# Kernel tuning notes

Hardware: AMD Instinct MI355X
Metric: run time of the kernel (lower is better)

The kernel has to match this reference:

```python
import jax, jax.numpy as jnp
import numpy as np

N, D, E = 32768, 128, 524288
B, L = 64, 512          # 64 graphs of 512 nodes
H, DH = 8, 16           # heads, head dim


def setup_inputs() -> dict:
    key = jax.random.key(0)
    ks = jax.random.split(key, 16)
    s = 0.02
    w = lambda k, shape: (jax.random.normal(k, shape, jnp.float32) * s)
    z = lambda *shape: jnp.zeros(shape, jnp.float32)
    o = lambda *shape: jnp.ones(shape, jnp.float32)
    return {
        "x": jax.random.normal(ks[0], (N, D), jnp.float32),
        "edge_index": jax.random.randint(ks[1], (2, E), 0, N, jnp.int32),
        "eps": jnp.zeros(()),
        "W_loc1": w(ks[2], (D, 2 * D)), "b_loc1": z(2 * D),
        "W_loc2": w(ks[3], (2 * D, D)), "b_loc2": z(D),
        "g1": o(D), "beta1": z(D),
        "Wq": w(ks[4], (D, D)), "bq": z(D),
        "Wk": w(ks[5], (D, D)), "bk": z(D),
        "Wv": w(ks[6], (D, D)), "bv": z(D),
        "Wo": w(ks[7], (D, D)), "bo": z(D),
        "g2": o(D), "beta2": z(D),
        "Wf1": w(ks[8], (D, 2 * D)), "bf1": z(2 * D),
        "Wf2": w(ks[9], (2 * D, D)), "bf2": z(D),
        "g3": o(D), "beta3": z(D),
    }


def _bn(x, g, b):
    # BatchNorm1d, training mode: batch stats over the node dimension
    m = x.mean(0)
    v = x.var(0)
    return (x - m) * jax.lax.rsqrt(v + 1e-5) * g + b


def reference(x, edge_index, eps, W_loc1, b_loc1, W_loc2, b_loc2, g1, beta1,
              Wq, bq, Wk, bk, Wv, bv, Wo, bo, g2, beta2,
              Wf1, bf1, Wf2, bf2, g3, beta3):
    src, dst = edge_index[0], edge_index[1]
    # --- local MPNN (GIN): sum-aggregate neighbours then MLP ---
    agg = jax.ops.segment_sum(x[src], dst, num_segments=N)          # [N, D]
    h = (1.0 + eps) * x + agg
    h = jax.nn.relu(h @ W_loc1 + b_loc1) @ W_loc2 + b_loc2
    h_local = _bn(x + h, g1, beta1)
    # --- global attention over each graph's (permuted) node sequence ---
    xd = x.reshape(B, L, D)
    q = (xd @ Wq + bq).reshape(B, L, H, DH)
    k = (xd @ Wk + bk).reshape(B, L, H, DH)
    v = (xd @ Wv + bv).reshape(B, L, H, DH)
    scores = jnp.einsum("blhd,bmhd->bhlm", q, k) / np.sqrt(DH)
    attn = jax.nn.softmax(scores, axis=-1)
    o = jnp.einsum("bhlm,bmhd->blhd", attn, v).reshape(B, L, D)
    o = (o @ Wo + bo).reshape(N, D)
    h_attn = _bn(x + o, g2, beta2)
    # --- combine + FFN block ---
    h = h_local + h_attn
    f = jax.nn.relu(h @ Wf1 + bf1) @ Wf2 + bf2
    return _bn(h + f, g3, beta3)
```

## Files before the change

kernel.cpp:

```cpp
#include <hip/hip_runtime.h>
#include <cstdint>
#include <cstddef>

typedef unsigned short u16;
typedef unsigned int u32;

using short8 = __attribute__((ext_vector_type(8))) short;
using f32x4  = __attribute__((ext_vector_type(4))) float;

__device__ __forceinline__ float b2f(u16 v) {
  union { u32 u; float f; } c; c.u = ((u32)v) << 16; return c.f;
}
__device__ __forceinline__ u16 f2b(float f) {
  union { float f; u32 u; } c; c.f = f;
  u32 u = c.u;
  u += 0x7fffu + ((u >> 16) & 1u);
  return (u16)(u >> 16);
}

__global__ __launch_bounds__(256)
void f2bf_kernel(const float* __restrict__ in, u16* __restrict__ outp) {
  int i = blockIdx.x * 256 + threadIdx.x;
  float2 v = *(const float2*)(in + (size_t)i * 2);
  *(u32*)(outp + (size_t)i * 2) = (u32)f2b(v.x) | ((u32)f2b(v.y) << 16);
}

__global__ __launch_bounds__(256)
void prep_kernel(const float* __restrict__ Wl1, const float* __restrict__ Wl2,
                 const float* __restrict__ Wq,  const float* __restrict__ Wk,
                 const float* __restrict__ Wv,  const float* __restrict__ Wo,
                 const float* __restrict__ Wf1, const float* __restrict__ Wf2,
                 const float* __restrict__ bl1, const float* __restrict__ bl2,
                 const float* __restrict__ bq,  const float* __restrict__ bk,
                 const float* __restrict__ bv,  const float* __restrict__ bo,
                 const float* __restrict__ bf1, const float* __restrict__ bf2,
                 u16* __restrict__ Bt, float* __restrict__ biasAll) {
  int idx = blockIdx.x * 256 + threadIdx.x;
  if (idx < 196608) {
    const float* W; int local, ks, N;
    if      (idx <  32768) { W = Wl1; local = idx;          ks = 7; N = 256; }
    else if (idx <  65536) { W = Wl2; local = idx - 32768;  ks = 8; N = 128; }
    else if (idx <  81920) { W = Wq;  local = idx - 65536;  ks = 7; N = 128; }
    else if (idx <  98304) { W = Wk;  local = idx - 81920;  ks = 7; N = 128; }
    else if (idx < 114688) { W = Wv;  local = idx - 98304;  ks = 7; N = 128; }
    else if (idx < 131072) { W = Wo;  local = idx - 114688; ks = 7; N = 128; }
    else if (idx < 163840) { W = Wf1; local = idx - 131072; ks = 7; N = 256; }
    else                   { W = Wf2; local = idx - 163840; ks = 8; N = 128; }
    int n = local >> ks, k = local & ((1 << ks) - 1);
    Bt[idx] = f2b(W[(size_t)k * N + n]);
  }
  int t = idx - 196608;
  if (t >= 0 && t < 1280) {
    float v;
    if      (t <  256) v = bl1[t];
    else if (t <  384) v = bl2[t - 256];
    else if (t <  512) v = bq[t - 384];
    else if (t <  640) v = bk[t - 512];
    else if (t <  768) v = bv[t - 640];
    else if (t <  896) v = bo[t - 768];
    else if (t < 1152) v = bf1[t - 896];
    else               v = bf2[t - 1152];
    biasAll[t] = v;
  }
}

__global__ void hist_kernel(const int* __restrict__ dst, int* __restrict__ deg, int E) {
  int i = blockIdx.x * 256 + threadIdx.x;
  if (i < E) atomicAdd(&deg[dst[i]], 1);
}

__global__ __launch_bounds__(256)
void scan1_kernel(const int* __restrict__ deg, int* __restrict__ bsum) {
  int t = threadIdx.x, b = blockIdx.x;
  int v = deg[b * 256 + t];
#pragma unroll
  for (int off = 1; off < 64; off <<= 1) v += __shfl_xor(v, off);
  __shared__ int wsum[4];
  if ((t & 63) == 0) wsum[t >> 6] = v;
  __syncthreads();
  if (t == 0) bsum[b] = wsum[0] + wsum[1] + wsum[2] + wsum[3];
}

__global__ void scan2_kernel(const int* __restrict__ bsum, int* __restrict__ boff,
                             int* __restrict__ rowptrN) {
  __shared__ int sh[128];
  int t = threadIdx.x;
  int v = bsum[t];
  sh[t] = v;
  __syncthreads();
  for (int off = 1; off < 128; off <<= 1) {
    int u = (t >= off) ? sh[t - off] : 0;
    __syncthreads();
    sh[t] += u;
    __syncthreads();
  }
  boff[t] = sh[t] - v;
  if (t == 127) *rowptrN = sh[127];
}

__global__ __launch_bounds__(256)
void scan3_kernel(const int* __restrict__ deg, const int* __restrict__ boff,
                  int* __restrict__ rowptr, int* __restrict__ cursor) {
  __shared__ int sh[256];
  int t = threadIdx.x, b = blockIdx.x;
  int idx = b * 256 + t;
  int v = deg[idx];
  sh[t] = v;
  __syncthreads();
  for (int off = 1; off < 256; off <<= 1) {
    int u = (t >= off) ? sh[t - off] : 0;
    __syncthreads();
    sh[t] += u;
    __syncthreads();
  }
  int ex = sh[t] - v + boff[b];
  rowptr[idx] = ex;
  cursor[idx] = ex;
}

__global__ void scatter_kernel(const int* __restrict__ src, const int* __restrict__ dst,
                               int* __restrict__ cursor, int* __restrict__ csr, int E) {
  int i = blockIdx.x * 256 + threadIdx.x;
  if (i < E) {
    int d = dst[i];
    int pos = atomicAdd(&cursor[d], 1);
    csr[pos] = src[i];
  }
}

__global__ __launch_bounds__(256)
void agg_kernel(const u16* __restrict__ xb, const float* __restrict__ x,
                const int* __restrict__ csr, const int* __restrict__ rowptr,
                const float* __restrict__ eps, u16* __restrict__ hin, int N) {
  int node = blockIdx.x * 4 + (threadIdx.x >> 6);
  if (node >= N) return;
  int lane = threadIdx.x & 63;
  float ep1 = 1.0f + eps[0];
  int s0 = rowptr[node], s1 = rowptr[node + 1];
  float a0 = 0.f, a1 = 0.f;
  int e = s0;
  for (; e + 4 <= s1; e += 4) {
    int i0 = csr[e], i1 = csr[e + 1], i2 = csr[e + 2], i3 = csr[e + 3];
    u32 w0 = *(const u32*)(xb + (size_t)i0 * 128 + lane * 2);
    u32 w1 = *(const u32*)(xb + (size_t)i1 * 128 + lane * 2);
    u32 w2 = *(const u32*)(xb + (size_t)i2 * 128 + lane * 2);
    u32 w3 = *(const u32*)(xb + (size_t)i3 * 128 + lane * 2);
    a0 += b2f((u16)w0) + b2f((u16)w1) + b2f((u16)w2) + b2f((u16)w3);
    a1 += b2f((u16)(w0 >> 16)) + b2f((u16)(w1 >> 16))
        + b2f((u16)(w2 >> 16)) + b2f((u16)(w3 >> 16));
  }
  for (; e < s1; e++) {
    int s = csr[e];
    u32 w = *(const u32*)(xb + (size_t)s * 128 + lane * 2);
    a0 += b2f((u16)w);
    a1 += b2f((u16)(w >> 16));
  }
  float2 xw = *(const float2*)(x + (size_t)node * 128 + lane * 2);
  a0 += ep1 * xw.x;
  a1 += ep1 * xw.y;
  *(u32*)(hin + (size_t)node * 128 + lane * 2) = (u32)f2b(a0) | ((u32)f2b(a1) << 16);
}

__global__ __launch_bounds__(256)
void gemm_fast(const u16* __restrict__ A, const u16* __restrict__ Bt,
               const float* __restrict__ bias, const float* __restrict__ residf,
               const u16* __restrict__ residb,
               u16* __restrict__ C0, u16* __restrict__ C1, u16* __restrict__ C2,
               float* __restrict__ ssum, float* __restrict__ ssq,
               int K, int ntshift, int relu, float scale0, int headmajor) {
  const int tid = threadIdx.x, wave = tid >> 6, lane = tid & 63;
  const int quad = lane >> 4, c = lane & 15;
  const int y = blockIdx.y;
  const int ti = y >> ntshift, nt = y & ((1 << ntshift) - 1);
  const int Nout = 32 << ntshift;
  const u16* Btp = Bt + (size_t)ti * Nout * K;
  const float* bp = bias + ti * Nout;
  u16* C = (ti == 0) ? C0 : ((ti == 1) ? C1 : C2);
  const float scl = (ti == 0) ? scale0 : 1.0f;
  const int row0 = blockIdx.x * 128 + wave * 32;
  const int col0 = nt * 32;

  const u16* Ap0 = A   + (size_t)(row0 + c) * K + quad * 8;
  const u16* Ap1 = Ap0 + (size_t)16 * K;
  const u16* Bp0 = Btp + (size_t)(col0 + c) * K + quad * 8;
  const u16* Bp1 = Bp0 + (size_t)16 * K;

  f32x4 acc[2][2];
#pragma unroll
  for (int i = 0; i < 2; i++)
#pragma unroll
    for (int j = 0; j < 2; j++)
#pragma unroll
      for (int r = 0; r < 4; r++) acc[i][j][r] = 0.f;

#pragma unroll 4
  for (int kc = 0; kc < K; kc += 32) {
    short8 a0 = *(const short8*)(Ap0 + kc);
    short8 a1 = *(const short8*)(Ap1 + kc);
    short8 b0 = *(const short8*)(Bp0 + kc);
    short8 b1 = *(const short8*)(Bp1 + kc);
    acc[0][0] = __builtin_amdgcn_mfma_f32_16x16x32_bf16(a0, b0, acc[0][0], 0, 0, 0);
    acc[0][1] = __builtin_amdgcn_mfma_f32_16x16x32_bf16(a0, b1, acc[0][1], 0, 0, 0);
    acc[1][0] = __builtin_amdgcn_mfma_f32_16x16x32_bf16(a1, b0, acc[1][0], 0, 0, 0);
    acc[1][1] = __builtin_amdgcn_mfma_f32_16x16x32_bf16(a1, b1, acc[1][1], 0, 0, 0);
  }

#pragma unroll
  for (int ci = 0; ci < 2; ci++) {
    int col = col0 + ci * 16 + c;
    float bv = bp[col];
    float sp = 0.f, qp = 0.f;
#pragma unroll
    for (int mi = 0; mi < 2; mi++) {
#pragma unroll
      for (int r = 0; r < 4; r++) {
        int m = row0 + mi * 16 + quad * 4 + r;
        float v = acc[mi][ci][r] + bv;
        if (relu) v = fmaxf(v, 0.f);
        if (residf) v += residf[(size_t)m * Nout + col];
        else if (residb) v += b2f(residb[(size_t)m * Nout + col]);
        v *= scl;
        size_t cidx;
        if (headmajor) {
          int bb = m >> 9, j = m & 511;
          cidx = (size_t)(bb * 8 + (col >> 4)) * 8192 + (size_t)j * 16 + (col & 15);
        } else {
          cidx = (size_t)m * Nout + col;
        }
        C[cidx] = f2b(v);
        sp += v; qp += v * v;
      }
    }
    if (ssum) {
      sp += __shfl_xor(sp, 16); sp += __shfl_xor(sp, 32);
      qp += __shfl_xor(qp, 16); qp += __shfl_xor(qp, 32);
      if (quad == 0) {
        atomicAdd(&ssum[col], sp);
        atomicAdd(&ssq[col], qp);
      }
    }
  }
}

__global__ __launch_bounds__(512)
void attn_kernel(const u16* __restrict__ Q, const u16* __restrict__ Km,
                 const u16* __restrict__ Vm, u16* __restrict__ O) {
  __shared__ __align__(16) u16 Ksh[512 * 24];
  __shared__ __align__(16) u16 Vt[16 * 520];
  __shared__ __align__(16) u16 Psh[8][16 * 40];
  const int bh = blockIdx.x >> 1, qhalf = blockIdx.x & 1;
  const int b = bh >> 3, hh = bh & 7;
  const size_t qkvbase = (size_t)bh * 8192;
  const size_t obase   = (size_t)b * 512 * 128 + hh * 16;
  const int tid = threadIdx.x;

  {
    int j = tid;
    short8 k0 = *(const short8*)(Km + qkvbase + (size_t)j * 16);
    short8 k1 = *(const short8*)(Km + qkvbase + (size_t)j * 16 + 8);
    short8 v0 = *(const short8*)(Vm + qkvbase + (size_t)j * 16);
    short8 v1 = *(const short8*)(Vm + qkvbase + (size_t)j * 16 + 8);
    *(short8*)&Ksh[j * 24]     = k0;
    *(short8*)&Ksh[j * 24 + 8] = k1;
    int jl = j & 31;
    int j2 = (j & ~31) | (((jl & 15) << 1) | (jl >> 4));
#pragma unroll
    for (int t = 0; t < 8; t++) Vt[t * 520 + j2] = (u16)v0[t];
#pragma unroll
    for (int t = 0; t < 8; t++) Vt[(8 + t) * 520 + j2] = (u16)v1[t];
  }
  __syncthreads();

  const int wave = tid >> 6, lane = tid & 63;
  const int quad = lane >> 4, c = lane & 15;
  u16* Pw = &Psh[wave][0];
  u32* Pw32 = (u32*)Pw;

  short8 ones;
#pragma unroll
  for (int i = 0; i < 8; i++) ones[i] = (short)0x3F80;
  const f32x4 zero = {0.f, 0.f, 0.f, 0.f};

  for (int qt = qhalf * 16 + wave; qt < (qhalf + 1) * 16; qt += 8) {
    short8 qfrag = (short8)0;
    if (quad < 2)
      qfrag = *(const short8*)(Q + qkvbase + (size_t)(qt * 16 + c) * 16 + quad * 8);

    f32x4 accO = zero, accL = zero;
    for (int jp = 0; jp < 16; jp++) {
      short8 kf0 = (short8)0, kf1 = (short8)0;
      if (quad < 2) {
        kf0 = *(const short8*)&Ksh[(jp * 32 + c) * 24 + quad * 8];
        kf1 = *(const short8*)&Ksh[(jp * 32 + 16 + c) * 24 + quad * 8];
      }
      f32x4 s0 = __builtin_amdgcn_mfma_f32_16x16x32_bf16(qfrag, kf0, zero, 0, 0, 0);
      f32x4 s1 = __builtin_amdgcn_mfma_f32_16x16x32_bf16(qfrag, kf1, zero, 0, 0, 0);
#pragma unroll
      for (int r = 0; r < 4; r++) {
        union { float f; u32 u; } u0, u1;
        u0.f = exp2f(s0[r]);
        u1.f = exp2f(s1[r]);
        Pw32[(quad * 4 + r) * 20 + c] = (u0.u >> 16) | (u1.u & 0xffff0000u);
      }
      short8 pf = *(const short8*)&Pw[c * 40 + quad * 8];
      short8 vf = *(const short8*)&Vt[c * 520 + jp * 32 + quad * 8];
      accO = __builtin_amdgcn_mfma_f32_16x16x32_bf16(pf, vf, accO, 0, 0, 0);
      accL = __builtin_amdgcn_mfma_f32_16x16x32_bf16(pf, ones, accL, 0, 0, 0);
    }
#pragma unroll
    for (int r = 0; r < 4; r++) {
      float o = accO[r] / accL[r];
      O[obase + (size_t)(qt * 16 + quad * 4 + r) * 128 + c] = f2b(o);
    }
  }
}

__global__ __launch_bounds__(256)
void combine_kernel(const u16* __restrict__ y1, const u16* __restrict__ y2,
                    const float* __restrict__ stats,
                    const float* __restrict__ g1, const float* __restrict__ be1,
                    const float* __restrict__ g2, const float* __restrict__ be2,
                    u16* __restrict__ hout, float invM) {
  int i = blockIdx.x * 256 + threadIdx.x;
  int e0 = i * 2;
  int c = e0 & 127;
  float sc1a, sh1a, sc1b, sh1b, sc2a, sh2a, sc2b, sh2b;
  {
    float m = stats[c] * invM, vv = stats[128 + c] * invM - m * m;
    sc1a = g1[c] * rsqrtf(vv + 1e-5f); sh1a = be1[c] - m * sc1a;
    m = stats[c + 1] * invM; vv = stats[129 + c] * invM - m * m;
    sc1b = g1[c + 1] * rsqrtf(vv + 1e-5f); sh1b = be1[c + 1] - m * sc1b;
    m = stats[256 + c] * invM; vv = stats[384 + c] * invM - m * m;
    sc2a = g2[c] * rsqrtf(vv + 1e-5f); sh2a = be2[c] - m * sc2a;
    m = stats[257 + c] * invM; vv = stats[385 + c] * invM - m * m;
    sc2b = g2[c + 1] * rsqrtf(vv + 1e-5f); sh2b = be2[c + 1] - m * sc2b;
  }
  u32 w1 = *(const u32*)(y1 + e0);
  u32 w2 = *(const u32*)(y2 + e0);
  float r0 = b2f((u16)w1) * sc1a + sh1a + b2f((u16)w2) * sc2a + sh2a;
  float r1 = b2f((u16)(w1 >> 16)) * sc1b + sh1b + b2f((u16)(w2 >> 16)) * sc2b + sh2b;
  *(u32*)(hout + e0) = (u32)f2b(r0) | ((u32)f2b(r1) << 16);
}

__global__ __launch_bounds__(256)
void norm_kernel(const u16* __restrict__ y3, const float* __restrict__ stats3,
                 const float* __restrict__ g3, const float* __restrict__ be3,
                 float* __restrict__ outp, float invM) {
  int i = blockIdx.x * 256 + threadIdx.x;
  int e0 = i * 2;
  int c = e0 & 127;
  float m = stats3[c] * invM, vv = stats3[128 + c] * invM - m * m;
  float sca = g3[c] * rsqrtf(vv + 1e-5f), sha = be3[c] - m * sca;
  m = stats3[c + 1] * invM; vv = stats3[129 + c] * invM - m * m;
  float scb = g3[c + 1] * rsqrtf(vv + 1e-5f), shb = be3[c + 1] - m * scb;
  u32 w = *(const u32*)(y3 + e0);
  float2 r;
  r.x = b2f((u16)w) * sca + sha;
  r.y = b2f((u16)(w >> 16)) * scb + shb;
  *(float2*)(outp + e0) = r;
}

extern "C" void kernel_launch(void* const* d_in, const int* in_sizes, int n_in,
                              void* d_out, int out_size, void* d_ws, size_t ws_size,
                              hipStream_t stream) {
  const float* x   = (const float*)d_in[0];
  const int*   ei  = (const int*)d_in[1];
  const float* eps = (const float*)d_in[2];
  const float* Wl1 = (const float*)d_in[3];  const float* bl1 = (const float*)d_in[4];
  const float* Wl2 = (const float*)d_in[5];  const float* bl2 = (const float*)d_in[6];
  const float* g1  = (const float*)d_in[7];  const float* be1 = (const float*)d_in[8];
  const float* Wq  = (const float*)d_in[9];  const float* bq  = (const float*)d_in[10];
  const float* Wk  = (const float*)d_in[11]; const float* bk  = (const float*)d_in[12];
  const float* Wv  = (const float*)d_in[13]; const float* bv  = (const float*)d_in[14];
  const float* Wo  = (const float*)d_in[15]; const float* bo  = (const float*)d_in[16];
  const float* g2  = (const float*)d_in[17]; const float* be2 = (const float*)d_in[18];
  const float* Wf1 = (const float*)d_in[19]; const float* bf1 = (const float*)d_in[20];
  const float* Wf2 = (const float*)d_in[21]; const float* bf2 = (const float*)d_in[22];
  const float* g3  = (const float*)d_in[23]; const float* be3 = (const float*)d_in[24];
  float* out = (float*)d_out;

  const int N = in_sizes[0] / 128;
  const int E = in_sizes[1] / 2;
  const size_t MB = 1048576;
  const float invM = 1.0f / (float)N;

  char* ws = (char*)d_ws;
  u16* hin = (u16*)(ws + 0);
  u16* t1  = (u16*)(ws + 8 * MB);
  int* deg    = (int*)(ws + 8 * MB);
  int* rowptr = (int*)(ws + 8 * MB + 256 * 1024);
  int* cursor = (int*)(ws + 8 * MB + 512 * 1024);
  int* csr    = (int*)(ws + 8 * MB + 768 * 1024);
  u16* qb  = (u16*)(ws + 24 * MB);
  u16* kb  = (u16*)(ws + 32 * MB);
  u16* vb  = (u16*)(ws + 40 * MB);
  u16* xb  = (u16*)(ws + 48 * MB);
  u16* y2  = xb;
  float* stats = (float*)(ws + 56 * MB);
  int* bsum = (int*)(ws + 56 * MB + 8192);
  int* boff = (int*)(ws + 56 * MB + 8192 + 512);
  u16* y1 = (u16*)d_out;
  u16*   BtAll   = (u16*)((char*)d_out + 8 * MB);
  float* biasAll = (float*)((char*)d_out + 8 * MB + 400 * 1024);

  hipMemsetAsync(deg, 0, (size_t)N * sizeof(int), stream);
  hipMemsetAsync(stats, 0, 6 * 128 * sizeof(float), stream);

  const int* srcv = ei;
  const int* dstv = ei + E;
  const float QSCL = 0.25f * 1.44269504088896f;

  prep_kernel<<<774, 256, 0, stream>>>(Wl1, Wl2, Wq, Wk, Wv, Wo, Wf1, Wf2,
                                       bl1, bl2, bq, bk, bv, bo, bf1, bf2,
                                       BtAll, biasAll);
  f2bf_kernel<<<(N * 128 / 2) / 256, 256, 0, stream>>>(x, xb);
  hist_kernel<<<(E + 255) / 256, 256, 0, stream>>>(dstv, deg, E);
  scan1_kernel<<<N / 256, 256, 0, stream>>>(deg, bsum);
  scan2_kernel<<<1, 128, 0, stream>>>(bsum, boff, rowptr + N);
  scan3_kernel<<<N / 256, 256, 0, stream>>>(deg, boff, rowptr, cursor);
  scatter_kernel<<<(E + 255) / 256, 256, 0, stream>>>(srcv, dstv, cursor, csr, E);
  agg_kernel<<<N / 4, 256, 0, stream>>>(xb, x, csr, rowptr, eps, hin, N);

  dim3 blk(256);
  gemm_fast<<<dim3(N / 128, 8), blk, 0, stream>>>(hin, BtAll + 0, biasAll + 0,
      nullptr, nullptr, t1, nullptr, nullptr, nullptr, nullptr, 128, 3, 1, 1.0f, 0);
  gemm_fast<<<dim3(N / 128, 4), blk, 0, stream>>>(t1, BtAll + 32768, biasAll + 256,
      x, nullptr, y1, nullptr, nullptr, stats + 0, stats + 128, 256, 2, 0, 1.0f, 0);
  gemm_fast<<<dim3(N / 128, 12), blk, 0, stream>>>(xb, BtAll + 65536, biasAll + 384,
      nullptr, nullptr, qb, kb, vb, nullptr, nullptr, 128, 2, 0, QSCL, 1);
  attn_kernel<<<(N / 512) * 8 * 2, dim3(512), 0, stream>>>(qb, kb, vb, hin);
  gemm_fast<<<dim3(N / 128, 4), blk, 0, stream>>>(hin, BtAll + 114688, biasAll + 768,
      x, nullptr, y2, nullptr, nullptr, stats + 256, stats + 384, 128, 2, 0, 1.0f, 0);
  combine_kernel<<<(N * 128 / 2) / 256, blk, 0, stream>>>(y1, y2, stats,
      g1, be1, g2, be2, qb, invM);
  gemm_fast<<<dim3(N / 128, 8), blk, 0, stream>>>(qb, BtAll + 131072, biasAll + 896,
      nullptr, nullptr, t1, nullptr, nullptr, nullptr, nullptr, 128, 3, 1, 1.0f, 0);
  gemm_fast<<<dim3(N / 128, 4), blk, 0, stream>>>(t1, BtAll + 163840, biasAll + 1152,
      nullptr, qb, kb, nullptr, nullptr, stats + 512, stats + 640, 256, 2, 0, 1.0f, 0);
  norm_kernel<<<(N * 128 / 2) / 256, blk, 0, stream>>>(kb, stats + 512, g3, be3, out, invM);
}
```

Measured before the change: 472.1 us.

## Shrink GEMM tiles to 16x16 per wave with templated K and bf16 residual

```diff
diff --git a/kernel.cpp b/kernel.cpp
--- a/kernel.cpp
+++ b/kernel.cpp
@@ -161,83 +161,66 @@
   *(u32*)(hin + (size_t)node * 128 + lane * 2) = (u32)f2b(a0) | ((u32)f2b(a1) << 16);
 }
 
+template<int K>
 __global__ __launch_bounds__(256)
 void gemm_fast(const u16* __restrict__ A, const u16* __restrict__ Bt,
-               const float* __restrict__ bias, const float* __restrict__ residf,
-               const u16* __restrict__ residb,
+               const float* __restrict__ bias, const u16* __restrict__ residb,
                u16* __restrict__ C0, u16* __restrict__ C1, u16* __restrict__ C2,
                float* __restrict__ ssum, float* __restrict__ ssq,
-               int K, int ntshift, int relu, float scale0, int headmajor) {
+               int ntshift, int relu, float scale0, int headmajor) {
   const int tid = threadIdx.x, wave = tid >> 6, lane = tid & 63;
   const int quad = lane >> 4, c = lane & 15;
   const int y = blockIdx.y;
   const int ti = y >> ntshift, nt = y & ((1 << ntshift) - 1);
-  const int Nout = 32 << ntshift;
+  const int Nout = 16 << ntshift;
   const u16* Btp = Bt + (size_t)ti * Nout * K;
   const float* bp = bias + ti * Nout;
   u16* C = (ti == 0) ? C0 : ((ti == 1) ? C1 : C2);
   const float scl = (ti == 0) ? scale0 : 1.0f;
-  const int row0 = blockIdx.x * 128 + wave * 32;
-  const int col0 = nt * 32;
-
-  const u16* Ap0 = A   + (size_t)(row0 + c) * K + quad * 8;
-  const u16* Ap1 = Ap0 + (size_t)16 * K;
-  const u16* Bp0 = Btp + (size_t)(col0 + c) * K + quad * 8;
-  const u16* Bp1 = Bp0 + (size_t)16 * K;
-
-  f32x4 acc[2][2];
-#pragma unroll
-  for (int i = 0; i < 2; i++)
-#pragma unroll
-    for (int j = 0; j < 2; j++)
-#pragma unroll
-      for (int r = 0; r < 4; r++) acc[i][j][r] = 0.f;
-
-#pragma unroll 4
-  for (int kc = 0; kc < K; kc += 32) {
-    short8 a0 = *(const short8*)(Ap0 + kc);
-    short8 a1 = *(const short8*)(Ap1 + kc);
-    short8 b0 = *(const short8*)(Bp0 + kc);
-    short8 b1 = *(const short8*)(Bp1 + kc);
-    acc[0][0] = __builtin_amdgcn_mfma_f32_16x16x32_bf16(a0, b0, acc[0][0], 0, 0, 0);
-    acc[0][1] = __builtin_amdgcn_mfma_f32_16x16x32_bf16(a0, b1, acc[0][1], 0, 0, 0);
-    acc[1][0] = __builtin_amdgcn_mfma_f32_16x16x32_bf16(a1, b0, acc[1][0], 0, 0, 0);
-    acc[1][1] = __builtin_amdgcn_mfma_f32_16x16x32_bf16(a1, b1, acc[1][1], 0, 0, 0);
-  }
-
-#pragma unroll
-  for (int ci = 0; ci < 2; ci++) {
-    int col = col0 + ci * 16 + c;
-    float bv = bp[col];
-    float sp = 0.f, qp = 0.f;
-#pragma unroll
-    for (int mi = 0; mi < 2; mi++) {
-#pragma unroll
-      for (int r = 0; r < 4; r++) {
-        int m = row0 + mi * 16 + quad * 4 + r;
-        float v = acc[mi][ci][r] + bv;
-        if (relu) v = fmaxf(v, 0.f);
-        if (residf) v += residf[(size_t)m * Nout + col];
-        else if (residb) v += b2f(residb[(size_t)m * Nout + col]);
-        v *= scl;
-        size_t cidx;
-        if (headmajor) {
-          int bb = m >> 9, j = m & 511;
-          cidx = (size_t)(bb * 8 + (col >> 4)) * 8192 + (size_t)j * 16 + (col & 15);
-        } else {
-          cidx = (size_t)m * Nout + col;
-        }
-        C[cidx] = f2b(v);
-        sp += v; qp += v * v;
-      }
+  const int row0 = blockIdx.x * 64 + wave * 16;
+  const int col0 = nt * 16;
+
+  const u16* Ap = A   + (size_t)(row0 + c) * K + quad * 8;
+  const u16* Bp = Btp + (size_t)(col0 + c) * K + quad * 8;
+
+  constexpr int NI = K / 32;
+  short8 af[NI], bf[NI];
+#pragma unroll
+  for (int i = 0; i < NI; i++) {
+    af[i] = *(const short8*)(Ap + i * 32);
+    bf[i] = *(const short8*)(Bp + i * 32);
+  }
+  f32x4 acc = {0.f, 0.f, 0.f, 0.f};
+#pragma unroll
+  for (int i = 0; i < NI; i++)
+    acc = __builtin_amdgcn_mfma_f32_16x16x32_bf16(af[i], bf[i], acc, 0, 0, 0);
+
+  const int col = col0 + c;
+  const float bv = bp[col];
+  float sp = 0.f, qp = 0.f;
+#pragma unroll
+  for (int r = 0; r < 4; r++) {
+    int m = row0 + quad * 4 + r;
+    float v = acc[r] + bv;
+    if (relu) v = fmaxf(v, 0.f);
+    if (residb) v += b2f(residb[(size_t)m * Nout + col]);
+    v *= scl;
+    size_t cidx;
+    if (headmajor) {
+      int bb = m >> 9, j = m & 511;
+      cidx = (size_t)(bb * 8 + (col >> 4)) * 8192 + (size_t)j * 16 + (col & 15);
+    } else {
+      cidx = (size_t)m * Nout + col;
     }
-    if (ssum) {
-      sp += __shfl_xor(sp, 16); sp += __shfl_xor(sp, 32);
-      qp += __shfl_xor(qp, 16); qp += __shfl_xor(qp, 32);
-      if (quad == 0) {
-        atomicAdd(&ssum[col], sp);
-        atomicAdd(&ssq[col], qp);
-      }
+    C[cidx] = f2b(v);
+    sp += v; qp += v * v;
+  }
+  if (ssum) {
+    sp += __shfl_xor(sp, 16); sp += __shfl_xor(sp, 32);
+    qp += __shfl_xor(qp, 16); qp += __shfl_xor(qp, 32);
+    if (quad == 0) {
+      atomicAdd(&ssum[col], sp);
+      atomicAdd(&ssq[col], qp);
     }
   }
 }
@@ -422,20 +405,20 @@
   agg_kernel<<<N / 4, 256, 0, stream>>>(xb, x, csr, rowptr, eps, hin, N);
 
   dim3 blk(256);
-  gemm_fast<<<dim3(N / 128, 8), blk, 0, stream>>>(hin, BtAll + 0, biasAll + 0,
-      nullptr, nullptr, t1, nullptr, nullptr, nullptr, nullptr, 128, 3, 1, 1.0f, 0);
-  gemm_fast<<<dim3(N / 128, 4), blk, 0, stream>>>(t1, BtAll + 32768, biasAll + 256,
-      x, nullptr, y1, nullptr, nullptr, stats + 0, stats + 128, 256, 2, 0, 1.0f, 0);
-  gemm_fast<<<dim3(N / 128, 12), blk, 0, stream>>>(xb, BtAll + 65536, biasAll + 384,
-      nullptr, nullptr, qb, kb, vb, nullptr, nullptr, 128, 2, 0, QSCL, 1);
+  gemm_fast<128><<<dim3(N / 64, 16), blk, 0, stream>>>(hin, BtAll + 0, biasAll + 0,
+      nullptr, t1, nullptr, nullptr, nullptr, nullptr, 4, 1, 1.0f, 0);
+  gemm_fast<256><<<dim3(N / 64, 8), blk, 0, stream>>>(t1, BtAll + 32768, biasAll + 256,
+      xb, y1, nullptr, nullptr, stats + 0, stats + 128, 3, 0, 1.0f, 0);
+  gemm_fast<128><<<dim3(N / 64, 24), blk, 0, stream>>>(xb, BtAll + 65536, biasAll + 384,
+      nullptr, qb, kb, vb, nullptr, nullptr, 3, 0, QSCL, 1);
   attn_kernel<<<(N / 512) * 8 * 2, dim3(512), 0, stream>>>(qb, kb, vb, hin);
-  gemm_fast<<<dim3(N / 128, 4), blk, 0, stream>>>(hin, BtAll + 114688, biasAll + 768,
-      x, nullptr, y2, nullptr, nullptr, stats + 256, stats + 384, 128, 2, 0, 1.0f, 0);
+  gemm_fast<128><<<dim3(N / 64, 8), blk, 0, stream>>>(hin, BtAll + 114688, biasAll + 768,
+      xb, y2, nullptr, nullptr, stats + 256, stats + 384, 3, 0, 1.0f, 0);
   combine_kernel<<<(N * 128 / 2) / 256, blk, 0, stream>>>(y1, y2, stats,
       g1, be1, g2, be2, qb, invM);
-  gemm_fast<<<dim3(N / 128, 8), blk, 0, stream>>>(qb, BtAll + 131072, biasAll + 896,
-      nullptr, nullptr, t1, nullptr, nullptr, nullptr, nullptr, 128, 3, 1, 1.0f, 0);
-  gemm_fast<<<dim3(N / 128, 4), blk, 0, stream>>>(t1, BtAll + 163840, biasAll + 1152,
-      nullptr, qb, kb, nullptr, nullptr, stats + 512, stats + 640, 256, 2, 0, 1.0f, 0);
+  gemm_fast<128><<<dim3(N / 64, 16), blk, 0, stream>>>(qb, BtAll + 131072, biasAll + 896,
+      nullptr, t1, nullptr, nullptr, nullptr, nullptr, 4, 1, 1.0f, 0);
+  gemm_fast<256><<<dim3(N / 64, 8), blk, 0, stream>>>(t1, BtAll + 163840, biasAll + 1152,
+      qb, kb, nullptr, nullptr, stats + 512, stats + 640, 3, 0, 1.0f, 0);
   norm_kernel<<<(N * 128 / 2) / 256, blk, 0, stream>>>(kb, stats + 512, g3, be3, out, invM);
 }
```

New measurement: 691.9 us. 1.47x slower.

## Store activations and weights in 16x32 tiled layout for coalesced MFMA fragment loads

Applied to the files above, without the earlier changes.

```diff
diff --git a/kernel.cpp b/kernel.cpp
--- a/kernel.cpp
+++ b/kernel.cpp
@@ -7,6 +7,10 @@
 
 using short8 = __attribute__((ext_vector_type(8))) short;
 using f32x4  = __attribute__((ext_vector_type(4))) float;
+
+__device__ __forceinline__ size_t taddr(int m, int n, int nc32) {
+  return ((size_t)(m >> 4) * nc32 + (n >> 5)) * 512 + (m & 15) * 32 + (n & 31);
+}
 
 __device__ __forceinline__ float b2f(u16 v) {
   union { u32 u; float f; } c; c.u = ((u32)v) << 16; return c.f;
@@ -21,8 +25,11 @@
 __global__ __launch_bounds__(256)
 void f2bf_kernel(const float* __restrict__ in, u16* __restrict__ outp) {
   int i = blockIdx.x * 256 + threadIdx.x;
-  float2 v = *(const float2*)(in + (size_t)i * 2);
-  *(u32*)(outp + (size_t)i * 2) = (u32)f2b(v.x) | ((u32)f2b(v.y) << 16);
+  int el = i * 2;
+  int m = ((el >> 11) << 4) | ((el >> 5) & 15);
+  int n = (((el >> 9) & 3) << 5) | (el & 31);
+  float2 v = *(const float2*)(in + (size_t)m * 128 + n);
+  *(u32*)(outp + el) = (u32)f2b(v.x) | ((u32)f2b(v.y) << 16);
 }
 
 __global__ __launch_bounds__(256)
@@ -37,16 +44,20 @@
                  u16* __restrict__ Bt, float* __restrict__ biasAll) {
   int idx = blockIdx.x * 256 + threadIdx.x;
   if (idx < 196608) {
-    const float* W; int local, ks, N;
-    if      (idx <  32768) { W = Wl1; local = idx;          ks = 7; N = 256; }
-    else if (idx <  65536) { W = Wl2; local = idx - 32768;  ks = 8; N = 128; }
-    else if (idx <  81920) { W = Wq;  local = idx - 65536;  ks = 7; N = 128; }
-    else if (idx <  98304) { W = Wk;  local = idx - 81920;  ks = 7; N = 128; }
-    else if (idx < 114688) { W = Wv;  local = idx - 98304;  ks = 7; N = 128; }
-    else if (idx < 131072) { W = Wo;  local = idx - 114688; ks = 7; N = 128; }
-    else if (idx < 163840) { W = Wf1; local = idx - 131072; ks = 7; N = 256; }
-    else                   { W = Wf2; local = idx - 163840; ks = 8; N = 128; }
-    int n = local >> ks, k = local & ((1 << ks) - 1);
+    const float* W; int local, K, N;
+    if      (idx <  32768) { W = Wl1; local = idx;          K = 128; N = 256; }
+    else if (idx <  65536) { W = Wl2; local = idx - 32768;  K = 256; N = 128; }
+    else if (idx <  81920) { W = Wq;  local = idx - 65536;  K = 128; N = 128; }
+    else if (idx <  98304) { W = Wk;  local = idx - 81920;  K = 128; N = 128; }
+    else if (idx < 114688) { W = Wv;  local = idx - 98304;  K = 128; N = 128; }
+    else if (idx < 131072) { W = Wo;  local = idx - 114688; K = 128; N = 128; }
+    else if (idx < 163840) { W = Wf1; local = idx - 131072; K = 128; N = 256; }
+    else                   { W = Wf2; local = idx - 163840; K = 256; N = 128; }
+    int ks2 = (K == 256) ? 3 : 2;
+    int tile = local >> 9, within = local & 511;
+    int nr = within >> 5, kc = within & 31;
+    int n = ((tile >> ks2) << 4) + nr;
+    int k = ((tile & ((1 << ks2) - 1)) << 5) + kc;
     Bt[idx] = f2b(W[(size_t)k * N + n]);
   }
   int t = idx - 196608;
@@ -135,55 +146,61 @@
   int node = blockIdx.x * 4 + (threadIdx.x >> 6);
   if (node >= N) return;
   int lane = threadIdx.x & 63;
+  int laneoff = (lane >> 4) * 512 + (lane & 15) * 2;
   float ep1 = 1.0f + eps[0];
   int s0 = rowptr[node], s1 = rowptr[node + 1];
   float a0 = 0.f, a1 = 0.f;
   int e = s0;
   for (; e + 4 <= s1; e += 4) {
     int i0 = csr[e], i1 = csr[e + 1], i2 = csr[e + 2], i3 = csr[e + 3];
-    u32 w0 = *(const u32*)(xb + (size_t)i0 * 128 + lane * 2);
-    u32 w1 = *(const u32*)(xb + (size_t)i1 * 128 + lane * 2);
-    u32 w2 = *(const u32*)(xb + (size_t)i2 * 128 + lane * 2);
-    u32 w3 = *(const u32*)(xb + (size_t)i3 * 128 + lane * 2);
+    u32 w0 = *(const u32*)(xb + (size_t)(i0 >> 4) * 2048 + (i0 & 15) * 32 + laneoff);
+    u32 w1 = *(const u32*)(xb + (size_t)(i1 >> 4) * 2048 + (i1 & 15) * 32 + laneoff);
+    u32 w2 = *(const u32*)(xb + (size_t)(i2 >> 4) * 2048 + (i2 & 15) * 32 + laneoff);
+    u32 w3 = *(const u32*)(xb + (size_t)(i3 >> 4) * 2048 + (i3 & 15) * 32 + laneoff);
     a0 += b2f((u16)w0) + b2f((u16)w1) + b2f((u16)w2) + b2f((u16)w3);
     a1 += b2f((u16)(w0 >> 16)) + b2f((u16)(w1 >> 16))
         + b2f((u16)(w2 >> 16)) + b2f((u16)(w3 >> 16));
   }
   for (; e < s1; e++) {
     int s = csr[e];
-    u32 w = *(const u32*)(xb + (size_t)s * 128 + lane * 2);
+    u32 w = *(const u32*)(xb + (size_t)(s >> 4) * 2048 + (s & 15) * 32 + laneoff);
     a0 += b2f((u16)w);
     a1 += b2f((u16)(w >> 16));
   }
   float2 xw = *(const float2*)(x + (size_t)node * 128 + lane * 2);
   a0 += ep1 * xw.x;
   a1 += ep1 * xw.y;
-  *(u32*)(hin + (size_t)node * 128 + lane * 2) = (u32)f2b(a0) | ((u32)f2b(a1) << 16);
-}
-
+  *(u32*)(hin + (size_t)(node >> 4) * 2048 + (node & 15) * 32 + laneoff)
+      = (u32)f2b(a0) | ((u32)f2b(a1) << 16);
+}
+
+template<int K>
 __global__ __launch_bounds__(256)
 void gemm_fast(const u16* __restrict__ A, const u16* __restrict__ Bt,
-               const float* __restrict__ bias, const float* __restrict__ residf,
-               const u16* __restrict__ residb,
+               const float* __restrict__ bias, const u16* __restrict__ residb,
                u16* __restrict__ C0, u16* __restrict__ C1, u16* __restrict__ C2,
                float* __restrict__ ssum, float* __restrict__ ssq,
-               int K, int ntshift, int relu, float scale0, int headmajor) {
+               int ntshift, int relu, float scale0, int headmajor) {
   const int tid = threadIdx.x, wave = tid >> 6, lane = tid & 63;
   const int quad = lane >> 4, c = lane & 15;
   const int y = blockIdx.y;
-  const int ti = y >> ntshift, nt = y & ((1 << ntshift) - 1);
+  const int ti = y >> ntshift, ntv = y & ((1 << ntshift) - 1);
   const int Nout = 32 << ntshift;
+  const int nc32 = 1 << (ntshift - 0) >> 0 ? (Nout >> 5) : 0;
+  constexpr int KT = K >> 5;
   const u16* Btp = Bt + (size_t)ti * Nout * K;
   const float* bp = bias + ti * Nout;
   u16* C = (ti == 0) ? C0 : ((ti == 1) ? C1 : C2);
   const float scl = (ti == 0) ? scale0 : 1.0f;
   const int row0 = blockIdx.x * 128 + wave * 32;
-  const int col0 = nt * 32;
-
-  const u16* Ap0 = A   + (size_t)(row0 + c) * K + quad * 8;
-  const u16* Ap1 = Ap0 + (size_t)16 * K;
-  const u16* Bp0 = Btp + (size_t)(col0 + c) * K + quad * 8;
-  const u16* Bp1 = Bp0 + (size_t)16 * K;
+  const int mt0 = row0 >> 4;
+  const int col0 = ntv * 32;
+  const int loff = c * 32 + quad * 8;
+
+  const u16* Ap0 = A   + (size_t)(mt0)     * KT * 512 + loff;
+  const u16* Ap1 = A   + (size_t)(mt0 + 1) * KT * 512 + loff;
+  const u16* Bp0 = Btp + (size_t)(ntv * 2)     * KT * 512 + loff;
+  const u16* Bp1 = Btp + (size_t)(ntv * 2 + 1) * KT * 512 + loff;
 
   f32x4 acc[2][2];
 #pragma unroll
@@ -193,12 +210,12 @@
 #pragma unroll
       for (int r = 0; r < 4; r++) acc[i][j][r] = 0.f;
 
-#pragma unroll 4
-  for (int kc = 0; kc < K; kc += 32) {
-    short8 a0 = *(const short8*)(Ap0 + kc);
-    short8 a1 = *(const short8*)(Ap1 + kc);
-    short8 b0 = *(const short8*)(Bp0 + kc);
-    short8 b1 = *(const short8*)(Bp1 + kc);
+#pragma unroll
+  for (int i = 0; i < KT; i++) {
+    short8 a0 = *(const short8*)(Ap0 + i * 512);
+    short8 a1 = *(const short8*)(Ap1 + i * 512);
+    short8 b0 = *(const short8*)(Bp0 + i * 512);
+    short8 b1 = *(const short8*)(Bp1 + i * 512);
     acc[0][0] = __builtin_amdgcn_mfma_f32_16x16x32_bf16(a0, b0, acc[0][0], 0, 0, 0);
     acc[0][1] = __builtin_amdgcn_mfma_f32_16x16x32_bf16(a0, b1, acc[0][1], 0, 0, 0);
     acc[1][0] = __builtin_amdgcn_mfma_f32_16x16x32_bf16(a1, b0, acc[1][0], 0, 0, 0);
@@ -217,15 +234,17 @@
         int m = row0 + mi * 16 + quad * 4 + r;
         float v = acc[mi][ci][r] + bv;
         if (relu) v = fmaxf(v, 0.f);
-        if (residf) v += residf[(size_t)m * Nout + col];
-        else if (residb) v += b2f(residb[(size_t)m * Nout + col]);
+        if (residb)
+          v += b2f(residb[((size_t)(mt0 + mi) * 4 + (col >> 5)) * 512
+                          + (quad * 4 + r) * 32 + (col & 31)]);
         v *= scl;
         size_t cidx;
         if (headmajor) {
           int bb = m >> 9, j = m & 511;
           cidx = (size_t)(bb * 8 + (col >> 4)) * 8192 + (size_t)j * 16 + (col & 15);
         } else {
-          cidx = (size_t)m * Nout + col;
+          cidx = ((size_t)(mt0 + mi) * nc32 + ntv) * 512
+               + (quad * 4 + r) * 32 + ci * 16 + c;
         }
         C[cidx] = f2b(v);
         sp += v; qp += v * v;
@@ -251,7 +270,6 @@
   const int bh = blockIdx.x >> 1, qhalf = blockIdx.x & 1;
   const int b = bh >> 3, hh = bh & 7;
   const size_t qkvbase = (size_t)bh * 8192;
-  const size_t obase   = (size_t)b * 512 * 128 + hh * 16;
   const int tid = threadIdx.x;
 
   {
@@ -310,7 +328,9 @@
 #pragma unroll
     for (int r = 0; r < 4; r++) {
       float o = accO[r] / accL[r];
-      O[obase + (size_t)(qt * 16 + quad * 4 + r) * 128 + c] = f2b(o);
+      size_t oidx = ((size_t)(b * 32 + qt) * 4 + (hh >> 1)) * 512
+                  + (quad * 4 + r) * 32 + (hh & 1) * 16 + c;
+      O[oidx] = f2b(o);
     }
   }
 }
@@ -323,7 +343,7 @@
                     u16* __restrict__ hout, float invM) {
   int i = blockIdx.x * 256 + threadIdx.x;
   int e0 = i * 2;
-  int c = e0 & 127;
+  int c = (((e0 >> 9) & 3) << 5) | (e0 & 31);
   float sc1a, sh1a, sc1b, sh1b, sc2a, sh2a, sc2b, sh2b;
   {
     float m = stats[c] * invM, vv = stats[128 + c] * invM - m * m;
@@ -348,16 +368,17 @@
                  float* __restrict__ outp, float invM) {
   int i = blockIdx.x * 256 + threadIdx.x;
   int e0 = i * 2;
-  int c = e0 & 127;
-  float m = stats3[c] * invM, vv = stats3[128 + c] * invM - m * m;
-  float sca = g3[c] * rsqrtf(vv + 1e-5f), sha = be3[c] - m * sca;
-  m = stats3[c + 1] * invM; vv = stats3[129 + c] * invM - m * m;
-  float scb = g3[c + 1] * rsqrtf(vv + 1e-5f), shb = be3[c + 1] - m * scb;
+  int m = ((e0 >> 11) << 4) | ((e0 >> 5) & 15);
+  int c = (((e0 >> 9) & 3) << 5) | (e0 & 31);
+  float mm = stats3[c] * invM, vv = stats3[128 + c] * invM - mm * mm;
+  float sca = g3[c] * rsqrtf(vv + 1e-5f), sha = be3[c] - mm * sca;
+  mm = stats3[c + 1] * invM; vv = stats3[129 + c] * invM - mm * mm;
+  float scb = g3[c + 1] * rsqrtf(vv + 1e-5f), shb = be3[c + 1] - mm * scb;
   u32 w = *(const u32*)(y3 + e0);
   float2 r;
   r.x = b2f((u16)w) * sca + sha;
   r.y = b2f((u16)(w >> 16)) * scb + shb;
-  *(float2*)(outp + e0) = r;
+  *(float2*)(outp + (size_t)m * 128 + c) = r;
 }
 
 extern "C" void kernel_launch(void* const* d_in, const int* in_sizes, int n_in,
@@ -422,20 +443,20 @@
   agg_kernel<<<N / 4, 256, 0, stream>>>(xb, x, csr, rowptr, eps, hin, N);
 
   dim3 blk(256);
-  gemm_fast<<<dim3(N / 128, 8), blk, 0, stream>>>(hin, BtAll + 0, biasAll + 0,
-      nullptr, nullptr, t1, nullptr, nullptr, nullptr, nullptr, 128, 3, 1, 1.0f, 0);
-  gemm_fast<<<dim3(N / 128, 4), blk, 0, stream>>>(t1, BtAll + 32768, biasAll + 256,
-      x, nullptr, y1, nullptr, nullptr, stats + 0, stats + 128, 256, 2, 0, 1.0f, 0);
-  gemm_fast<<<dim3(N / 128, 12), blk, 0, stream>>>(xb, BtAll + 65536, biasAll + 384,
-      nullptr, nullptr, qb, kb, vb, nullptr, nullptr, 128, 2, 0, QSCL, 1);
+  gemm_fast<128><<<dim3(N / 128, 8), blk, 0, stream>>>(hin, BtAll + 0, biasAll + 0,
+      nullptr, t1, nullptr, nullptr, nullptr, nullptr, 3, 1, 1.0f, 0);
+  gemm_fast<256><<<dim3(N / 128, 4), blk, 0, stream>>>(t1, BtAll + 32768, biasAll + 256,
+      xb, y1, nullptr, nullptr, stats + 0, stats + 128, 2, 0, 1.0f, 0);
+  gemm_fast<128><<<dim3(N / 128, 12), blk, 0, stream>>>(xb, BtAll + 65536, biasAll + 384,
+      nullptr, qb, kb, vb, nullptr, nullptr, 2, 0, QSCL, 1);
   attn_kernel<<<(N / 512) * 8 * 2, dim3(512), 0, stream>>>(qb, kb, vb, hin);
-  gemm_fast<<<dim3(N / 128, 4), blk, 0, stream>>>(hin, BtAll + 114688, biasAll + 768,
-      x, nullptr, y2, nullptr, nullptr, stats + 256, stats + 384, 128, 2, 0, 1.0f, 0);
+  gemm_fast<128><<<dim3(N / 128, 4), blk, 0, stream>>>(hin, BtAll + 114688, biasAll + 768,
+      xb, y2, nullptr, nullptr, stats + 256, stats + 384, 2, 0, 1.0f, 0);
   combine_kernel<<<(N * 128 / 2) / 256, blk, 0, stream>>>(y1, y2, stats,
       g1, be1, g2, be2, qb, invM);
-  gemm_fast<<<dim3(N / 128, 8), blk, 0, stream>>>(qb, BtAll + 131072, biasAll + 896,
-      nullptr, nullptr, t1, nullptr, nullptr, nullptr, nullptr, 128, 3, 1, 1.0f, 0);
-  gemm_fast<<<dim3(N / 128, 4), blk, 0, stream>>>(t1, BtAll + 163840, biasAll + 1152,
-      nullptr, qb, kb, nullptr, nullptr, stats + 512, stats + 640, 256, 2, 0, 1.0f, 0);
+  gemm_fast<128><<<dim3(N / 128, 8), blk, 0, stream>>>(qb, BtAll + 131072, biasAll + 896,
+      nullptr, t1, nullptr, nullptr, nullptr, nullptr, 3, 1, 1.0f, 0);
+  gemm_fast<256><<<dim3(N / 128, 4), blk, 0, stream>>>(t1, BtAll + 163840, biasAll + 1152,
+      qb, kb, nullptr, nullptr, stats + 512, stats + 640, 2, 0, 1.0f, 0);
   norm_kernel<<<(N * 128 / 2) / 256, blk, 0, stream>>>(kb, stats + 512, g3, be3, out, invM);
 }
```

Result: faster. 430.3 us (-8.9%).
